# Kernel tuning notes

Hardware: AMD Instinct MI355X
Metric: run time of the kernel (lower is better)

Reference implementation:

```python
import math
import jax, jax.numpy as jnp
import numpy as np

EMBED_LEN = 512  # self.dk in the torch module (used for scaling, NOT the head dim)


def setup_inputs() -> dict:
    key = jax.random.key(0)
    kq, kk, kv = jax.random.split(key, 3)
    B, H, S, D = 2, 8, 4096, 64
    queries = jax.random.normal(kq, (B, H, S, D), dtype=jnp.float32)
    keys = jax.random.normal(kk, (B, H, S, D), dtype=jnp.float32)
    # NOTE: values enters as [B, S, H, D]; forward transposes dims (1,2).
    values = jax.random.normal(kv, (B, S, H, D), dtype=jnp.float32)
    return {"queries": queries, "keys": keys, "values": values}


def reference(queries, keys, values):
    # compatibility = Q @ K^T / sqrt(dk), dk = embed_len (512), mask=None branch
    scores = jnp.einsum("bhqd,bhkd->bhqk", queries, keys) / math.sqrt(EMBED_LEN)
    attn = jax.nn.softmax(scores, axis=3)
    # torch.transpose(values, 1, 2): [B,S,H,D] -> [B,H,S,D]
    v = jnp.swapaxes(values, 1, 2)
    return jnp.einsum("bhqk,bhkd->bhqd", attn, v)
```

## Files before the change

### kernel.cpp

```cpp
#include <hip/hip_runtime.h>

typedef __attribute__((ext_vector_type(8))) short bf16x8;
typedef __attribute__((ext_vector_type(4))) short s16x4;
typedef __attribute__((ext_vector_type(4))) float f32x4;

#define MFMA16 __builtin_amdgcn_mfma_f32_16x16x32_bf16

#if __has_builtin(__builtin_amdgcn_exp2f)
__device__ __forceinline__ float exp2_raw(float x) { return __builtin_amdgcn_exp2f(x); }
#else
__device__ __forceinline__ float exp2_raw(float x) {
    float r;
    asm volatile("v_exp_f32 %0, %1" : "=v"(r) : "v"(x));
    return r;
}
#endif

__device__ __forceinline__ short bf16s(float f) {
    __bf16 h = (__bf16)f;
    return __builtin_bit_cast(short, h);
}

__device__ __forceinline__ void gload16(const char* g, char* l) {
    __builtin_amdgcn_global_load_lds(
        (const __attribute__((address_space(1))) unsigned int*)g,
        (__attribute__((address_space(3))) unsigned int*)l, 16, 0, 0);
}

__global__ __launch_bounds__(256) void prep_k(const float* __restrict__ K,
                                              char* __restrict__ Kimg) {
    const int bid = blockIdx.x;
    const int t = threadIdx.x;
    const int c = t & 3, r = t >> 2;
    char* dst = Kimg + (size_t)bid * 8192;
    const float* src = K + (size_t)bid * 4096 + (size_t)r * 64 + c * 16;
    float e[16];
    *(float4*)(e)      = *(const float4*)(src);
    *(float4*)(e + 4)  = *(const float4*)(src + 4);
    *(float4*)(e + 8)  = *(const float4*)(src + 8);
    *(float4*)(e + 12) = *(const float4*)(src + 12);
#pragma unroll
    for (int lg = 0; lg < 4; ++lg) {
        s16x4 wv;
#pragma unroll
        for (int j = 0; j < 4; ++j) wv[j] = bf16s(e[lg * 4 + j]);
        const unsigned f = (unsigned)((((c >> 1) * 4 + lg) ^ (r & 7)));
        *(s16x4*)(dst + r * 128 + f * 16 + (c & 1) * 8) = wv;
    }
}

__global__ __launch_bounds__(256) void prep_v(const float* __restrict__ V,
                                              char* __restrict__ Vimg) {
    const int bid = blockIdx.x;
    const int head = bid >> 6, it = bid & 63;
    const int b = head >> 3, h = head & 7;
    const int t = threadIdx.x;
    const int d = t & 63, f0 = t >> 6;
    char* dst = Vimg + (size_t)bid * 8192;
#pragma unroll
    for (int ff = 0; ff < 2; ++ff) {
        const int f = f0 + ff * 4;
        const int hh = f >> 2, lg = f & 3;
        const int kv0 = hh * 32 + lg * 4;
        const float* src = V + ((size_t)b * 4096 + it * 64 + kv0) * 512 + h * 64 + d;
        bf16x8 wv;
#pragma unroll
        for (int j = 0; j < 4; ++j) wv[j]     = bf16s(src[(size_t)j * 512]);
#pragma unroll
        for (int j = 0; j < 4; ++j) wv[4 + j] = bf16s(src[(size_t)(16 + j) * 512]);
        *(bf16x8*)(dst + d * 128 + (unsigned)((f ^ (d & 7)) * 16)) = wv;
    }
}

__global__ __launch_bounds__(256, 2)
void sdpa_fa_kernel(const float* __restrict__ Q, const char* __restrict__ Kimg,
                    const char* __restrict__ Vimg, float* __restrict__ O) {
    __shared__ __align__(16) char LDS[65536];

    const int bid  = blockIdx.x;
    const int xcd  = bid & 7;
    const int idx  = bid >> 3;
    const int head = xcd + 8 * (idx >> 5);
    const int qt   = idx & 31;
    const int hb   = head * 64;

    const int t   = threadIdx.x;
    const int w   = t >> 6;
    const int qg  = w >> 1;
    const int kvg = w & 1;
    const int l   = t & 63;
    const int lg  = l >> 4;
    const int lc  = l & 15;
    const int lc7 = lc & 7;

    const float C1 = (float)(1.4426950408889634 / 22.627416997969522);

    bf16x8 qf[4][2];
#pragma unroll
    for (int qi = 0; qi < 4; ++qi) {
        const int qrow = qt * 128 + qg * 64 + qi * 16 + lc;
        const float* qp = Q + ((size_t)head * 4096 + qrow) * 64;
#pragma unroll
        for (int half = 0; half < 2; ++half) {
            bf16x8 f;
#pragma unroll
            for (int j = 0; j < 4; ++j) {
                f[j]     = bf16s(qp[half * 32 + lg * 4 + j] * C1);
                f[4 + j] = bf16s(qp[half * 32 + 16 + lg * 4 + j] * C1);
            }
            qf[qi][half] = f;
        }
    }

    bf16x8 ones;
#pragma unroll
    for (int j = 0; j < 8; ++j) ones[j] = (short)0x3F80;

    f32x4 Oa[4][4];
    f32x4 ls[4];
#pragma unroll
    for (int qi = 0; qi < 4; ++qi) {
        ls[qi] = (f32x4){0.f, 0.f, 0.f, 0.f};
#pragma unroll
        for (int dt = 0; dt < 4; ++dt) Oa[qi][dt] = (f32x4){0.f, 0.f, 0.f, 0.f};
    }

    const char* gimg = (w < 2) ? Kimg : Vimg;
    const char* gbase = gimg + (size_t)(hb + (w & 1)) * 8192 + l * 16;
    auto stage = [&](int it, int buf) {
        const char* g = gbase + (size_t)it * 16384;
        char* lb = LDS + buf * 32768 + w * 8192;
#pragma unroll
        for (int i = 0; i < 8; ++i) gload16(g + i * 1024, lb + i * 1024);
    };

    auto compute = [&](const char* Kb, const char* Vb) {
        bf16x8 kf[4][2];
#pragma unroll
        for (int g = 0; g < 4; ++g) {
            const unsigned ro = (unsigned)((g * 16 + lc) * 128);
            kf[g][0] = *(const bf16x8*)(Kb + ro + (unsigned)(((0 + lg) ^ lc7) * 16));
            kf[g][1] = *(const bf16x8*)(Kb + ro + (unsigned)(((4 + lg) ^ lc7) * 16));
        }
        f32x4 st[4][4];
#pragma unroll
        for (int g = 0; g < 4; ++g)
#pragma unroll
            for (int qi = 0; qi < 4; ++qi) {
                f32x4 a = (f32x4){0.f, 0.f, 0.f, 0.f};
                a = MFMA16(kf[g][0], qf[qi][0], a, 0, 0, 0);
                a = MFMA16(kf[g][1], qf[qi][1], a, 0, 0, 0);
                st[qi][g] = a;
            }

#pragma unroll
        for (int qi = 0; qi < 4; ++qi)
#pragma unroll
            for (int g = 0; g < 4; ++g)
#pragma unroll
                for (int r = 0; r < 4; ++r)
                    st[qi][g][r] = exp2_raw(st[qi][g][r]);

        bf16x8 pfr[4][2];
#pragma unroll
        for (int qi = 0; qi < 4; ++qi)
#pragma unroll
            for (int hh = 0; hh < 2; ++hh) {
                bf16x8 f;
#pragma unroll
                for (int j = 0; j < 4; ++j) {
                    f[j]     = bf16s(st[qi][hh * 2][j]);
                    f[4 + j] = bf16s(st[qi][hh * 2 + 1][j]);
                }
                pfr[qi][hh] = f;
            }

#pragma unroll
        for (int qi = 0; qi < 4; ++qi) {
            ls[qi] = MFMA16(pfr[qi][0], ones, ls[qi], 0, 0, 0);
            ls[qi] = MFMA16(pfr[qi][1], ones, ls[qi], 0, 0, 0);
        }
        bf16x8 vf[4][2];
#pragma unroll
        for (int dt = 0; dt < 4; ++dt) {
            const unsigned ro = (unsigned)((dt * 16 + lc) * 128);
            vf[dt][0] = *(const bf16x8*)(Vb + ro + (unsigned)(((0 + lg) ^ lc7) * 16));
            vf[dt][1] = *(const bf16x8*)(Vb + ro + (unsigned)(((4 + lg) ^ lc7) * 16));
        }
#pragma unroll
        for (int dt = 0; dt < 4; ++dt)
#pragma unroll
            for (int qi = 0; qi < 4; ++qi) {
                Oa[qi][dt] = MFMA16(pfr[qi][0], vf[dt][0], Oa[qi][dt], 0, 0, 0);
                Oa[qi][dt] = MFMA16(pfr[qi][1], vf[dt][1], Oa[qi][dt], 0, 0, 0);
            }
    };

    const char* K0 = LDS + kvg * 8192;
    const char* V0 = LDS + 16384 + kvg * 8192;
    const char* K1 = LDS + 32768 + kvg * 8192;
    const char* V1 = LDS + 32768 + 16384 + kvg * 8192;

    stage(0, 0);
    __syncthreads();

#pragma unroll 1
    for (int itp = 0; itp < 16; ++itp) {
        const int it0 = itp * 2;
        stage(it0 + 1, 1);
        compute(K0, V0);
        __syncthreads();
        if (it0 + 2 < 32) stage(it0 + 2, 0);
        compute(K1, V1);
        __syncthreads();
    }

    float* EP = (float*)LDS;
    float* LR = (float*)LDS + 128 * 66;

    if (kvg == 1) {
#pragma unroll
        for (int qi = 0; qi < 4; ++qi) {
#pragma unroll
            for (int dt = 0; dt < 4; ++dt)
#pragma unroll
                for (int r = 0; r < 4; ++r)
                    EP[(qg * 64 + qi * 16 + lg * 4 + r) * 66 + dt * 16 + lc] = Oa[qi][dt][r];
            if (lc == 0)
#pragma unroll
                for (int r = 0; r < 4; ++r) LR[qg * 64 + qi * 16 + lg * 4 + r] = ls[qi][r];
        }
    }
    __syncthreads();
    if (kvg == 0) {
#pragma unroll
        for (int qi = 0; qi < 4; ++qi) {
#pragma unroll
            for (int r = 0; r < 4; ++r) {
                const int qloc = qg * 64 + qi * 16 + lg * 4 + r;
                const float tot = ls[qi][r] + LR[qloc];
                const float inv = 1.0f / tot;
                float* og = O + ((size_t)head * 4096 + qt * 128 + qloc) * 64 + lc;
#pragma unroll
                for (int dt = 0; dt < 4; ++dt)
                    og[dt * 16] = (Oa[qi][dt][r] + EP[qloc * 66 + dt * 16 + lc]) * inv;
            }
        }
    }
}

extern "C" void kernel_launch(void* const* d_in, const int* in_sizes, int n_in,
                              void* d_out, int out_size, void* d_ws, size_t ws_size,
                              hipStream_t stream) {
    const float* Q = (const float*)d_in[0];
    const float* K = (const float*)d_in[1];
    const float* V = (const float*)d_in[2];
    float* Out = (float*)d_out;
    char* Kimg = (char*)d_ws;
    char* Vimg = (char*)d_ws + (size_t)8388608;
    prep_k<<<dim3(1024), dim3(256), 0, stream>>>(K, Kimg);
    prep_v<<<dim3(1024), dim3(256), 0, stream>>>(V, Vimg);
    sdpa_fa_kernel<<<dim3(512), dim3(256), 0, stream>>>(Q, Kimg, Vimg, Out);
}
```

Baseline: 88.16 us.

## Split per-tile compute into two halves to overlap exp with MFMA

Splits the 64-key tile inside compute into two 32-key halves. The exp2 and bf16 packing of one half are interleaved with the QK^T MFMAs of the other half and with the PV MFMAs of the first half. The aim is to hide transcendental (VALU) latency behind matrix-core work within a single wave instead of running the phases back to back. The summation order is unchanged in effect, but register pressure and instruction scheduling shift, which could hurt occupancy.

New measurement: 85.81 us. -2.7%, faster.

```diff
diff --git a/kernel.cpp b/kernel.cpp
--- a/kernel.cpp
+++ b/kernel.cpp
@@ -135,51 +135,55 @@
     };
 
     auto compute = [&](const char* Kb, const char* Vb) {
-        bf16x8 kf[4][2];
-#pragma unroll
-        for (int g = 0; g < 4; ++g) {
-            const unsigned ro = (unsigned)((g * 16 + lc) * 128);
-            kf[g][0] = *(const bf16x8*)(Kb + ro + (unsigned)(((0 + lg) ^ lc7) * 16));
-            kf[g][1] = *(const bf16x8*)(Kb + ro + (unsigned)(((4 + lg) ^ lc7) * 16));
-        }
-        f32x4 st[4][4];
-#pragma unroll
-        for (int g = 0; g < 4; ++g)
+        bf16x8 kf0[2][2];
+#pragma unroll
+        for (int g2 = 0; g2 < 2; ++g2) {
+            const unsigned ro = (unsigned)((g2 * 16 + lc) * 128);
+            kf0[g2][0] = *(const bf16x8*)(Kb + ro + (unsigned)(((0 + lg) ^ lc7) * 16));
+            kf0[g2][1] = *(const bf16x8*)(Kb + ro + (unsigned)(((4 + lg) ^ lc7) * 16));
+        }
+        f32x4 st0[4][2];
+#pragma unroll
+        for (int g2 = 0; g2 < 2; ++g2)
 #pragma unroll
             for (int qi = 0; qi < 4; ++qi) {
                 f32x4 a = (f32x4){0.f, 0.f, 0.f, 0.f};
-                a = MFMA16(kf[g][0], qf[qi][0], a, 0, 0, 0);
-                a = MFMA16(kf[g][1], qf[qi][1], a, 0, 0, 0);
-                st[qi][g] = a;
-            }
-
-#pragma unroll
-        for (int qi = 0; qi < 4; ++qi)
-#pragma unroll
-            for (int g = 0; g < 4; ++g)
-#pragma unroll
-                for (int r = 0; r < 4; ++r)
-                    st[qi][g][r] = exp2_raw(st[qi][g][r]);
-
-        bf16x8 pfr[4][2];
-#pragma unroll
-        for (int qi = 0; qi < 4; ++qi)
-#pragma unroll
-            for (int hh = 0; hh < 2; ++hh) {
-                bf16x8 f;
-#pragma unroll
-                for (int j = 0; j < 4; ++j) {
-                    f[j]     = bf16s(st[qi][hh * 2][j]);
-                    f[4 + j] = bf16s(st[qi][hh * 2 + 1][j]);
-                }
-                pfr[qi][hh] = f;
-            }
-
-#pragma unroll
-        for (int qi = 0; qi < 4; ++qi) {
-            ls[qi] = MFMA16(pfr[qi][0], ones, ls[qi], 0, 0, 0);
-            ls[qi] = MFMA16(pfr[qi][1], ones, ls[qi], 0, 0, 0);
-        }
+                a = MFMA16(kf0[g2][0], qf[qi][0], a, 0, 0, 0);
+                a = MFMA16(kf0[g2][1], qf[qi][1], a, 0, 0, 0);
+                st0[qi][g2] = a;
+            }
+
+        bf16x8 kf1[2][2];
+#pragma unroll
+        for (int g2 = 0; g2 < 2; ++g2) {
+            const unsigned ro = (unsigned)(((g2 + 2) * 16 + lc) * 128);
+            kf1[g2][0] = *(const bf16x8*)(Kb + ro + (unsigned)(((0 + lg) ^ lc7) * 16));
+            kf1[g2][1] = *(const bf16x8*)(Kb + ro + (unsigned)(((4 + lg) ^ lc7) * 16));
+        }
+        f32x4 st1[4][2];
+#pragma unroll
+        for (int g2 = 0; g2 < 2; ++g2)
+#pragma unroll
+            for (int qi = 0; qi < 4; ++qi) {
+                f32x4 a = (f32x4){0.f, 0.f, 0.f, 0.f};
+                a = MFMA16(kf1[g2][0], qf[qi][0], a, 0, 0, 0);
+                a = MFMA16(kf1[g2][1], qf[qi][1], a, 0, 0, 0);
+                st1[qi][g2] = a;
+#pragma unroll
+                for (int r = 0; r < 4; ++r) st0[qi][g2][r] = exp2_raw(st0[qi][g2][r]);
+            }
+        bf16x8 pfr0[4];
+#pragma unroll
+        for (int qi = 0; qi < 4; ++qi) {
+            bf16x8 f;
+#pragma unroll
+            for (int j = 0; j < 4; ++j) {
+                f[j]     = bf16s(st0[qi][0][j]);
+                f[4 + j] = bf16s(st0[qi][1][j]);
+            }
+            pfr0[qi] = f;
+        }
+
         bf16x8 vf[4][2];
 #pragma unroll
         for (int dt = 0; dt < 4; ++dt) {
@@ -188,12 +192,36 @@
             vf[dt][1] = *(const bf16x8*)(Vb + ro + (unsigned)(((4 + lg) ^ lc7) * 16));
         }
 #pragma unroll
-        for (int dt = 0; dt < 4; ++dt)
-#pragma unroll
-            for (int qi = 0; qi < 4; ++qi) {
-                Oa[qi][dt] = MFMA16(pfr[qi][0], vf[dt][0], Oa[qi][dt], 0, 0, 0);
-                Oa[qi][dt] = MFMA16(pfr[qi][1], vf[dt][1], Oa[qi][dt], 0, 0, 0);
-            }
+        for (int qi = 0; qi < 4; ++qi) {
+            ls[qi] = MFMA16(pfr0[qi], ones, ls[qi], 0, 0, 0);
+#pragma unroll
+            for (int r = 0; r < 4; ++r) st1[qi][0][r] = exp2_raw(st1[qi][0][r]);
+            Oa[qi][0] = MFMA16(pfr0[qi], vf[0][0], Oa[qi][0], 0, 0, 0);
+            Oa[qi][1] = MFMA16(pfr0[qi], vf[1][0], Oa[qi][1], 0, 0, 0);
+#pragma unroll
+            for (int r = 0; r < 4; ++r) st1[qi][1][r] = exp2_raw(st1[qi][1][r]);
+            Oa[qi][2] = MFMA16(pfr0[qi], vf[2][0], Oa[qi][2], 0, 0, 0);
+            Oa[qi][3] = MFMA16(pfr0[qi], vf[3][0], Oa[qi][3], 0, 0, 0);
+        }
+        bf16x8 pfr1[4];
+#pragma unroll
+        for (int qi = 0; qi < 4; ++qi) {
+            bf16x8 f;
+#pragma unroll
+            for (int j = 0; j < 4; ++j) {
+                f[j]     = bf16s(st1[qi][0][j]);
+                f[4 + j] = bf16s(st1[qi][1][j]);
+            }
+            pfr1[qi] = f;
+        }
+
+#pragma unroll
+        for (int qi = 0; qi < 4; ++qi) {
+            ls[qi] = MFMA16(pfr1[qi], ones, ls[qi], 0, 0, 0);
+#pragma unroll
+            for (int dt = 0; dt < 4; ++dt)
+                Oa[qi][dt] = MFMA16(pfr1[qi], vf[dt][1], Oa[qi][dt], 0, 0, 0);
+        }
     };
 
     const char* K0 = LDS + kvg * 8192;
```
